# Performance work log

Hardware: AMD Instinct MI355X
Metric: run time of the kernel (lower is better)

## Reference

```python
import jax, jax.numpy as jnp
import numpy as np

N_EMBD = 2048
DIM_ATT = 2048
HEAD_SIZE = 64
N_HEAD = DIM_ATT // HEAD_SIZE
N_LAYER = 24
LAYER_ID = 12
CHUNK_LEN = 512
HEAD_DIV = 8
B = 4
TT = 4096


def _init_params():
    ratio_0_to_1 = LAYER_ID / (N_LAYER - 1)
    ratio_1_to_almost0 = 1.0 - LAYER_ID / N_LAYER
    ddd = (np.arange(N_EMBD) / N_EMBD).reshape(1, 1, N_EMBD).astype(np.float32)
    time_mix_k = np.power(ddd, ratio_1_to_almost0)
    time_mix_v = np.power(ddd, ratio_1_to_almost0) + 0.3 * ratio_0_to_1
    time_mix_r = np.power(ddd, 0.5 * ratio_1_to_almost0)
    time_mix_g = np.power(ddd, 0.5 * ratio_1_to_almost0)
    h = np.arange(N_HEAD, dtype=np.float32)
    time_decay = -8 + 7 * (h / (N_HEAD - 1)) ** (0.7 + 1.3 * ratio_0_to_1)
    time_faaaa = np.full(N_HEAD, 0.05, dtype=np.float32)
    return (jnp.asarray(time_mix_k), jnp.asarray(time_mix_v), jnp.asarray(time_mix_r),
            jnp.asarray(time_mix_g), jnp.asarray(time_decay.astype(np.float32)), jnp.asarray(time_faaaa))


def setup_inputs() -> dict:
    key = jax.random.key(0)
    ks = jax.random.split(key, 8)
    scale = 1.0 / np.sqrt(N_EMBD)
    x = jax.random.normal(ks[0], (B, TT, N_EMBD), dtype=jnp.float32)
    W_r = jax.random.normal(ks[1], (N_EMBD, DIM_ATT), dtype=jnp.float32) * scale
    W_k = jax.random.normal(ks[2], (N_EMBD, DIM_ATT), dtype=jnp.float32) * scale
    W_v = jax.random.normal(ks[3], (N_EMBD, DIM_ATT), dtype=jnp.float32) * scale
    W_g = jax.random.normal(ks[4], (N_EMBD, DIM_ATT), dtype=jnp.float32) * scale
    W_o = jax.random.normal(ks[5], (DIM_ATT, N_EMBD), dtype=jnp.float32) * scale
    ln_gamma = jnp.ones((DIM_ATT,), dtype=jnp.float32)
    ln_beta = jnp.zeros((DIM_ATT,), dtype=jnp.float32)
    tmk, tmv, tmr, tmg, tdecay, tfaaaa = _init_params()
    state0 = jnp.zeros((B, N_HEAD, HEAD_SIZE, HEAD_SIZE), dtype=jnp.float32)
    return dict(x=x, W_r=W_r, W_k=W_k, W_v=W_v, W_g=W_g, W_o=W_o,
                ln_gamma=ln_gamma, ln_beta=ln_beta,
                time_mix_k=tmk, time_mix_v=tmv, time_mix_r=tmr, time_mix_g=tmg,
                time_decay=tdecay, time_faaaa=tfaaaa, state0=state0)


def _group_norm(x, gamma, beta, num_groups, eps=1e-5):
    # x: [N, C]
    N, C = x.shape
    xg = x.reshape(N, num_groups, C // num_groups)
    mean = xg.mean(axis=-1, keepdims=True)
    var = xg.var(axis=-1, keepdims=True)
    xn = (xg - mean) * jax.lax.rsqrt(var + eps)
    return xn.reshape(N, C) * gamma + beta


def _decay_mats(time_decay, time_faaaa, T):
    w1 = jnp.exp(-jnp.exp(time_decay))[:, None]              # [H,1]
    u = time_faaaa[:, None]                                  # [H,1]
    ws = (w1 ** T).reshape(1, N_HEAD, 1, 1)                  # [1,H,1,1]
    ind = jnp.arange(T - 1, -1, -1, dtype=jnp.float32)[None, :]  # [1,T]
    w = w1 ** ind                                            # [H,T] decays T-1..0
    wk = w.reshape(1, N_HEAD, 1, T)
    wb = jnp.flip(wk, axis=-1).swapaxes(-2, -1)              # [1,H,T,1]
    wcat = jnp.concatenate([w[:, 1:], u], axis=1)            # [H,T]
    wpad = jnp.pad(wcat, ((0, 0), (0, T)))                   # [H,2T]
    wt = jnp.tile(wpad, (1, T))[:, :-T].reshape(N_HEAD, T, 2 * T - 1)
    wmat = wt[:, :, T - 1:].reshape(1, N_HEAD, T, T)         # intra-chunk matrix
    return wmat, wk, wb, ws


def reference(x, W_r, W_k, W_v, W_g, W_o, ln_gamma, ln_beta,
              time_mix_k, time_mix_v, time_mix_r, time_mix_g,
              time_decay, time_faaaa, state0):
    Bx, T_total, C = x.shape
    H, S = N_HEAD, HEAD_SIZE
    T = min(CHUNK_LEN, T_total)

    # time shift: prepend zeros (initial TimeShift state)
    xx = jnp.concatenate([jnp.zeros((Bx, 1, C), x.dtype), x[:, :-1, :]], axis=1)
    xk = x * time_mix_k + xx * (1 - time_mix_k)
    xv = x * time_mix_v + xx * (1 - time_mix_v)
    xr = x * time_mix_r + xx * (1 - time_mix_r)
    xg = x * time_mix_g + xx * (1 - time_mix_g)

    r = (xr @ W_r).reshape(Bx, T_total, H, S).transpose(0, 2, 1, 3)   # [B,H,TT,S]
    k = (xk @ W_k).reshape(Bx, T_total, H, S).transpose(0, 2, 3, 1)   # [B,H,S,TT]
    v = (xv @ W_v).reshape(Bx, T_total, H, S).transpose(0, 2, 1, 3)   # [B,H,TT,S]
    g = jax.nn.silu(xg @ W_g)                                         # [B,TT,C]

    wmat, wk, wb, ws = _decay_mats(time_decay, time_faaaa, T)
    wmat = wmat.astype(r.dtype); wk = wk.astype(r.dtype)
    wb = wb.astype(r.dtype); ws = ws.astype(r.dtype)

    nchunks = T_total // T
    # reshape into chunks: [nchunks, B, H, T, S]
    rc = r.reshape(Bx, H, nchunks, T, S).transpose(2, 0, 1, 3, 4)
    kc = k.reshape(Bx, H, S, nchunks, T).transpose(3, 0, 1, 2, 4)   # [n,B,H,S,T]
    vc = v.reshape(Bx, H, nchunks, T, S).transpose(2, 0, 1, 3, 4)

    def step(s, inp):
        rr, kk, vv = inp  # [B,H,T,S], [B,H,S,T], [B,H,T,S]
        att = (rr @ kk) * wmat                  # [B,H,T,T]
        out = att @ vv + (rr @ s) * wb          # [B,H,T,S]
        s_new = ws * s + (kk * wk) @ vv         # [B,H,S,S]
        return s_new, out

    s_final, xs = jax.lax.scan(step, state0.astype(r.dtype), (rc, kc, vc))
    # xs: [n,B,H,T,S] -> [B,H,TT,S]
    xout = xs.transpose(1, 2, 0, 3, 4).reshape(Bx, H, T_total, S)
    xout = xout.transpose(0, 2, 1, 3).reshape(Bx * T_total, H * S)
    xout = _group_norm(xout / HEAD_DIV, ln_gamma, ln_beta, H)
    xout = xout.reshape(Bx, T_total, H * S) * g
    return xout @ W_o
```

## Files before the change

kernel.cpp:

```cpp
#include <hip/hip_runtime.h>

typedef unsigned short u16;
typedef short short8 __attribute__((ext_vector_type(8)));
typedef float f32x4 __attribute__((ext_vector_type(4)));

struct __attribute__((aligned(8), may_alias)) U2 { unsigned int x, y; };
struct __attribute__((aligned(16), may_alias)) U4 { unsigned int x, y, z, w; };
struct __attribute__((aligned(16), may_alias)) F4 { float x, y, z, w; };

__device__ __forceinline__ float bf2f(u16 h) {
    union { unsigned int u; float f; } x; x.u = ((unsigned int)h) << 16; return x.f;
}
__device__ __forceinline__ u16 f2bf(float f) {
    union { float f; unsigned int u; } x; x.f = f;
    return (u16)((x.u + 0x7FFFu + ((x.u >> 16) & 1u)) >> 16);
}
__device__ __forceinline__ short8 lds8(const u16* p) {
    union { U2 q[2]; short8 s; } u;
    u.q[0] = *(const U2*)p;
    u.q[1] = *(const U2*)(p + 4);
    return u.s;
}
__device__ __forceinline__ void gl_lds16(const u16* g, u16* l) {
    __builtin_amdgcn_global_load_lds(
        (const __attribute__((address_space(1))) void*)g,
        (__attribute__((address_space(3))) void*)l, 16, 0, 0);
}

__global__ void transpose5(const float* __restrict__ s0, const float* __restrict__ s1,
                           const float* __restrict__ s2, const float* __restrict__ s3,
                           const float* __restrict__ s4,
                           u16* __restrict__ d0, u16* __restrict__ d1,
                           u16* __restrict__ d2, u16* __restrict__ d3,
                           u16* __restrict__ d4)
{
    const float* S; u16* D;
    switch (blockIdx.z) {
        case 0: S = s0; D = d0; break;
        case 1: S = s1; D = d1; break;
        case 2: S = s2; D = d2; break;
        case 3: S = s3; D = d3; break;
        default: S = s4; D = d4; break;
    }
    __shared__ float tile[32][33];
    int tx = threadIdx.x, ty = threadIdx.y;
    int bx = blockIdx.x * 32, by = blockIdx.y * 32;
    #pragma unroll
    for (int i = 0; i < 32; i += 8)
        tile[ty + i][tx] = S[(size_t)(by + ty + i) * 2048 + bx + tx];
    __syncthreads();
    #pragma unroll
    for (int i = 0; i < 32; i += 8)
        D[(size_t)(bx + ty + i) * 2048 + by + tx] = f2bf(tile[tx][ty + i]);
}

__global__ __launch_bounds__(256, 4) void mix_rows(
    const float* __restrict__ x, const float* __restrict__ tmix, u16* __restrict__ out)
{
    const int t = blockIdx.x;
    const int c = threadIdx.x * 8;
    const float* xp = x + (size_t)t * 2048 + c;
    const bool first = (t & 4095) == 0;
    F4 a0 = *(const F4*)xp, a1 = *(const F4*)(xp + 4);
    F4 p0 = {0.f, 0.f, 0.f, 0.f}, p1 = {0.f, 0.f, 0.f, 0.f};
    if (!first) { p0 = *(const F4*)(xp - 2048); p1 = *(const F4*)(xp - 2048 + 4); }
    F4 t0 = *(const F4*)(tmix + c), t1 = *(const F4*)(tmix + c + 4);
    float xc[8] = {a0.x, a0.y, a0.z, a0.w, a1.x, a1.y, a1.z, a1.w};
    float xq[8] = {p0.x, p0.y, p0.z, p0.w, p1.x, p1.y, p1.z, p1.w};
    float tm[8] = {t0.x, t0.y, t0.z, t0.w, t1.x, t1.y, t1.z, t1.w};
    union { u16 s[8]; U4 v; } ov;
    #pragma unroll
    for (int e = 0; e < 8; ++e)
        ov.s[e] = f2bf(xq[e] + tm[e] * (xc[e] - xq[e]));
    *(U4*)(out + (size_t)t * 2048 + c) = ov.v;
}

__device__ __forceinline__ void storeC(u16* p, float v) { *p = f2bf(v); }
__device__ __forceinline__ void storeC(float* p, float v) { *p = v; }

template <typename CT>
__global__ __launch_bounds__(256, 1) void gemm_bt(
    const u16* __restrict__ A, const u16* __restrict__ Bt, CT* __restrict__ C,
    int M, int N, int K)
{
    __shared__ u16 As[128][32];
    __shared__ u16 Bs[128][32];
    const int tid = threadIdx.x;
    const int lane = tid & 63, wv = tid >> 6;
    const int quad = lane >> 4, l16 = lane & 15;
    const int wm = (wv >> 1) * 64, wn = (wv & 1) * 64;
    const int bm = blockIdx.x * 128, bn = blockIdx.y * 128;

    const int sr = tid >> 2, ss = tid & 3;
    const u16* ga0 = A + (size_t)(bm + sr) * K + ss * 8;
    const u16* ga1 = A + (size_t)(bm + sr + 64) * K + ss * 8;
    const u16* gb0 = Bt + (size_t)(bn + sr) * K + ss * 8;
    const u16* gb1 = Bt + (size_t)(bn + sr + 64) * K + ss * 8;
    u16* la0 = &As[sr][ss * 8];
    u16* la1 = &As[sr + 64][ss * 8];
    u16* lb0 = &Bs[sr][ss * 8];
    u16* lb1 = &Bs[sr + 64][ss * 8];

    f32x4 acc[4][4];
    const f32x4 zero4 = {0.f, 0.f, 0.f, 0.f};
    #pragma unroll
    for (int i = 0; i < 4; ++i)
        #pragma unroll
        for (int j = 0; j < 4; ++j) acc[i][j] = zero4;

    for (int k0 = 0; k0 < K; k0 += 32) {
        __syncthreads();
        gl_lds16(ga0 + k0, la0);
        gl_lds16(ga1 + k0, la1);
        gl_lds16(gb0 + k0, lb0);
        gl_lds16(gb1 + k0, lb1);
        __syncthreads();
        short8 af[4], bfv[4];
        #pragma unroll
        for (int mt = 0; mt < 4; ++mt) af[mt] = lds8(&As[wm + mt * 16 + l16][quad * 8]);
        #pragma unroll
        for (int nt = 0; nt < 4; ++nt) bfv[nt] = lds8(&Bs[wn + nt * 16 + l16][quad * 8]);
        #pragma unroll
        for (int mt = 0; mt < 4; ++mt)
            #pragma unroll
            for (int nt = 0; nt < 4; ++nt)
                acc[mt][nt] = __builtin_amdgcn_mfma_f32_16x16x32_bf16(
                    af[mt], bfv[nt], acc[mt][nt], 0, 0, 0);
    }
    #pragma unroll
    for (int mt = 0; mt < 4; ++mt)
        #pragma unroll
        for (int nt = 0; nt < 4; ++nt)
            #pragma unroll
            for (int r = 0; r < 4; ++r) {
                int row = bm + wm + mt * 16 + quad * 4 + r;
                int col = bn + wn + nt * 16 + l16;
                storeC(&C[(size_t)row * N + col], acc[mt][nt][r]);
            }
}

__global__ __launch_bounds__(512, 1) void wkv_kernel(
    const u16* __restrict__ Rb, const u16* __restrict__ Kb,
    const u16* __restrict__ Vb, const u16* __restrict__ Gb,
    const float* __restrict__ td, const float* __restrict__ tf,
    const float* __restrict__ gamma, const float* __restrict__ beta,
    const float* __restrict__ st0, u16* __restrict__ Xout)
{
    __shared__ u16 kt[64][72];
    __shared__ u16 vtT[64][72];
    __shared__ u16 Pb[8][64][40];
    __shared__ float wpow[513];
    u16* stT = &Pb[0][0][0];

    const int blk = blockIdx.x;
    const int b = blk >> 5, h = blk & 31;
    const int tid = threadIdx.x;
    const int w = tid >> 6, lane = tid & 63;
    const int quad = lane >> 4, l16 = lane & 15;

    const float E = expf(td[h]);
    const float u = tf[h];
    for (int p = tid; p <= 512; p += 512) wpow[p] = expf(-(float)p * E);

    const int mtS = w >> 1;
    const int ntS0 = (w & 1) * 2;
    f32x4 stReg[2];
    {
        const float* sp = st0 + (((size_t)b * 32 + h) << 12);
        #pragma unroll
        for (int q = 0; q < 2; ++q)
            #pragma unroll
            for (int r = 0; r < 4; ++r) {
                int s1 = mtS * 16 + quad * 4 + r;
                int s2 = (ntS0 + q) * 16 + l16;
                stReg[q][r] = sp[s1 * 64 + s2];
            }
    }

    const size_t rowbase = ((size_t)b * 4096) * 2048 + (size_t)h * 64;
    const f32x4 zero4 = {0.f, 0.f, 0.f, 0.f};
    __syncthreads();

    for (int c = 0; c < 8; ++c) {
        const int t0 = c * 512;
        __syncthreads();
        #pragma unroll
        for (int q = 0; q < 2; ++q)
            #pragma unroll
            for (int r = 0; r < 4; ++r) {
                int s1 = mtS * 16 + quad * 4 + r;
                int s2 = (ntS0 + q) * 16 + l16;
                stT[s2 * 72 + s1] = f2bf(stReg[q][r]);
            }
        __syncthreads();

        short8 ar[4][2];
        #pragma unroll
        for (int mt = 0; mt < 4; ++mt)
            #pragma unroll
            for (int ks = 0; ks < 2; ++ks) {
                int t = t0 + w * 64 + mt * 16 + l16;
                const u16* p = Rb + rowbase + (size_t)t * 2048 + ks * 32 + quad * 8;
                union { U4 v; short8 s; } uu; uu.v = *(const U4*)p;
                ar[mt][ks] = uu.s;
            }

        f32x4 acc[4][4];
        #pragma unroll
        for (int i = 0; i < 4; ++i)
            #pragma unroll
            for (int j = 0; j < 4; ++j) acc[i][j] = zero4;
        #pragma unroll
        for (int ks = 0; ks < 2; ++ks)
            #pragma unroll
            for (int nt = 0; nt < 4; ++nt) {
                short8 bs = lds8(&stT[(nt * 16 + l16) * 72 + ks * 32 + quad * 8]);
                #pragma unroll
                for (int mt = 0; mt < 4; ++mt)
                    acc[mt][nt] = __builtin_amdgcn_mfma_f32_16x16x32_bf16(
                        ar[mt][ks], bs, acc[mt][nt], 0, 0, 0);
            }
        #pragma unroll
        for (int mt = 0; mt < 4; ++mt)
            #pragma unroll
            for (int r = 0; r < 4; ++r) {
                float f = wpow[w * 64 + mt * 16 + quad * 4 + r];
                #pragma unroll
                for (int nt = 0; nt < 4; ++nt) acc[mt][nt][r] *= f;
            }

        f32x4 sacc[2] = {zero4, zero4};

        for (int J = 0; J < 8; ++J) {
            __syncthreads();
            {
                int row = tid >> 3, seg = tid & 7;
                size_t goff = rowbase + (size_t)(t0 + J * 64 + row) * 2048 + seg * 8;
                union { U4 v; u16 s[8]; } kv, vv;
                kv.v = *(const U4*)(Kb + goff);
                vv.v = *(const U4*)(Vb + goff);
                *(U4*)&kt[row][seg * 8] = kv.v;
                #pragma unroll
                for (int e = 0; e < 8; ++e) vtT[seg * 8 + e][row] = vv.s[e];
            }
            __syncthreads();
            if (w >= J) {
                #pragma unroll
                for (int half = 0; half < 2; ++half) {
                    #pragma unroll
                    for (int jt2 = 0; jt2 < 2; ++jt2) {
                        int jt = half * 2 + jt2;
                        short8 bk0 = lds8(&kt[jt * 16 + l16][quad * 8]);
                        short8 bk1 = lds8(&kt[jt * 16 + l16][32 + quad * 8]);
                        #pragma unroll
                        for (int mt = 0; mt < 4; ++mt) {
                            f32x4 s4 = zero4;
                            s4 = __builtin_amdgcn_mfma_f32_16x16x32_bf16(ar[mt][0], bk0, s4, 0, 0, 0);
                            s4 = __builtin_amdgcn_mfma_f32_16x16x32_bf16(ar[mt][1], bk1, s4, 0, 0, 0);
                            int ibase = w * 64 + mt * 16 + quad * 4;
                            int j = J * 64 + jt * 16 + l16;
                            #pragma unroll
                            for (int r = 0; r < 4; ++r) {
                                int i = ibase + r;
                                float f = (j < i) ? wpow[i - j - 1] : ((j == i) ? u : 0.f);
                                Pb[w][mt * 16 + quad * 4 + r][jt2 * 16 + l16] = f2bf(s4[r] * f);
                            }
                        }
                    }
                    __builtin_amdgcn_wave_barrier();
                    short8 ap[4];
                    #pragma unroll
                    for (int mt = 0; mt < 4; ++mt)
                        ap[mt] = lds8(&Pb[w][mt * 16 + l16][quad * 8]);
                    #pragma unroll
                    for (int nt = 0; nt < 4; ++nt) {
                        short8 bv = lds8(&vtT[nt * 16 + l16][half * 32 + quad * 8]);
                        #pragma unroll
                        for (int mt = 0; mt < 4; ++mt)
                            acc[mt][nt] = __builtin_amdgcn_mfma_f32_16x16x32_bf16(
                                ap[mt], bv, acc[mt][nt], 0, 0, 0);
                    }
                }
            }
            {
                short8 aS[2];
                #pragma unroll
                for (int ks = 0; ks < 2; ++ks) {
                    union { short8 s; u16 us[8]; } t8;
                    #pragma unroll
                    for (int jj = 0; jj < 8; ++jj) {
                        int tl = ks * 32 + quad * 8 + jj;
                        float f = bf2f(kt[tl][mtS * 16 + l16]) * wpow[511 - (J * 64 + tl)];
                        t8.us[jj] = f2bf(f);
                    }
                    aS[ks] = t8.s;
                }
                #pragma unroll
                for (int q = 0; q < 2; ++q) {
                    short8 bv0 = lds8(&vtT[(ntS0 + q) * 16 + l16][quad * 8]);
                    short8 bv1 = lds8(&vtT[(ntS0 + q) * 16 + l16][32 + quad * 8]);
                    sacc[q] = __builtin_amdgcn_mfma_f32_16x16x32_bf16(aS[0], bv0, sacc[q], 0, 0, 0);
                    sacc[q] = __builtin_amdgcn_mfma_f32_16x16x32_bf16(aS[1], bv1, sacc[q], 0, 0, 0);
                }
            }
        }

        {
            float wsT = wpow[512];
            #pragma unroll
            for (int q = 0; q < 2; ++q)
                #pragma unroll
                for (int r = 0; r < 4; ++r)
                    stReg[q][r] = wsT * stReg[q][r] + sacc[q][r];
        }

        #pragma unroll
        for (int mt = 0; mt < 4; ++mt) {
            float rsum[4], rsq[4];
            #pragma unroll
            for (int r = 0; r < 4; ++r) {
                float s = 0.f, sq = 0.f;
                #pragma unroll
                for (int nt = 0; nt < 4; ++nt) {
                    float v = acc[mt][nt][r];
                    s += v; sq += v * v;
                }
                rsum[r] = s; rsq[r] = sq;
            }
            #pragma unroll
            for (int off = 1; off < 16; off <<= 1)
                #pragma unroll
                for (int r = 0; r < 4; ++r) {
                    rsum[r] += __shfl_xor(rsum[r], off);
                    rsq[r] += __shfl_xor(rsq[r], off);
                }
            #pragma unroll
            for (int r = 0; r < 4; ++r) {
                float mean = rsum[r] * (1.f / 512.f);
                float var = rsq[r] * (1.f / 4096.f) - mean * mean;
                float rstd = rsqrtf(var + 1e-5f);
                int tg = t0 + w * 64 + mt * 16 + quad * 4 + r;
                size_t obase = rowbase + (size_t)tg * 2048;
                #pragma unroll
                for (int nt = 0; nt < 4; ++nt) {
                    int ch = nt * 16 + l16;
                    float y = acc[mt][nt][r] * 0.125f;
                    float xn = (y - mean) * rstd * gamma[h * 64 + ch] + beta[h * 64 + ch];
                    float gl = bf2f(Gb[obase + ch]);
                    float sg = gl / (1.f + expf(-gl));
                    Xout[obase + ch] = f2bf(xn * sg);
                }
            }
        }
    }
}

extern "C" void kernel_launch(void* const* d_in, const int* in_sizes, int n_in,
                              void* d_out, int out_size, void* d_ws, size_t ws_size,
                              hipStream_t stream)
{
    const float* x   = (const float*)d_in[0];
    const float* Wr  = (const float*)d_in[1];
    const float* Wk  = (const float*)d_in[2];
    const float* Wv  = (const float*)d_in[3];
    const float* Wg  = (const float*)d_in[4];
    const float* Wo  = (const float*)d_in[5];
    const float* gam = (const float*)d_in[6];
    const float* bet = (const float*)d_in[7];
    const float* tmk = (const float*)d_in[8];
    const float* tmv = (const float*)d_in[9];
    const float* tmr = (const float*)d_in[10];
    const float* tmg = (const float*)d_in[11];
    const float* td  = (const float*)d_in[12];
    const float* tf  = (const float*)d_in[13];
    const float* st0 = (const float*)d_in[14];
    float* out = (float*)d_out;

    char* ws = (char*)d_ws;
    const size_t WSZ = (size_t)2048 * 2048 * 2;
    const size_t ASZ = (size_t)16384 * 2048 * 2;
    u16* WtR = (u16*)(ws + 0 * WSZ);
    u16* WtK = (u16*)(ws + 1 * WSZ);
    u16* WtV = (u16*)(ws + 2 * WSZ);
    u16* WtG = (u16*)(ws + 3 * WSZ);
    u16* WtO = (u16*)(ws + 4 * WSZ);
    char* act = ws + 5 * WSZ;
    u16* rb = (u16*)(act + 0 * ASZ);
    u16* kb = (u16*)(act + 1 * ASZ);
    u16* vb = (u16*)(act + 2 * ASZ);
    u16* gb = (u16*)(act + 3 * ASZ);
    u16* xo = gb;

    u16* mixA = (u16*)d_out;

    transpose5<<<dim3(64, 64, 5), dim3(32, 8), 0, stream>>>(
        Wr, Wk, Wv, Wg, Wo, WtR, WtK, WtV, WtG, WtO);

    dim3 ggrid(128, 16), gblk(256);
    dim3 mgrid(16384), mblk(256);

    mix_rows<<<mgrid, mblk, 0, stream>>>(x, tmr, mixA);
    gemm_bt<u16><<<ggrid, gblk, 0, stream>>>(mixA, WtR, rb, 16384, 2048, 2048);
    mix_rows<<<mgrid, mblk, 0, stream>>>(x, tmk, mixA);
    gemm_bt<u16><<<ggrid, gblk, 0, stream>>>(mixA, WtK, kb, 16384, 2048, 2048);
    mix_rows<<<mgrid, mblk, 0, stream>>>(x, tmv, mixA);
    gemm_bt<u16><<<ggrid, gblk, 0, stream>>>(mixA, WtV, vb, 16384, 2048, 2048);
    mix_rows<<<mgrid, mblk, 0, stream>>>(x, tmg, mixA);
    gemm_bt<u16><<<ggrid, gblk, 0, stream>>>(mixA, WtG, gb, 16384, 2048, 2048);

    wkv_kernel<<<dim3(128), dim3(512), 0, stream>>>(
        rb, kb, vb, gb, td, tf, gam, bet, st0, xo);

    gemm_bt<float><<<ggrid, gblk, 0, stream>>>(xo, WtO, out, 16384, 2048, 2048);
}
```

Before: 1.838 ms.

## Split WKV into chunk-parallel state, scan, and output kernels; pair mix kernels

The serial WKV kernel ran only 128 blocks (one per batch-head) that walked eight chunks in sequence. It is replaced by three kernels. The first computes each chunk's state contribution in parallel over 1024 blocks, the second runs a small scan that combines them with the initial state, and the third computes the chunk outputs in parallel over 1024 blocks. The aim is to fill the GPU instead of leaving most compute units idle during the recurrent section, at the cost of extra global traffic for the intermediate states. Separately, the token-shift mix kernels now produce two mixed inputs per launch, halving the reads of x.

```diff
diff --git a/kernel.cpp b/kernel.cpp
--- a/kernel.cpp
+++ b/kernel.cpp
@@ -54,8 +54,9 @@
         D[(size_t)(bx + ty + i) * 2048 + by + tx] = f2bf(tile[tx][ty + i]);
 }
 
-__global__ __launch_bounds__(256, 4) void mix_rows(
-    const float* __restrict__ x, const float* __restrict__ tmix, u16* __restrict__ out)
+__global__ __launch_bounds__(256, 4) void mix2_rows(
+    const float* __restrict__ x, const float* __restrict__ tmA,
+    const float* __restrict__ tmB, u16* __restrict__ outA, u16* __restrict__ outB)
 {
     const int t = blockIdx.x;
     const int c = threadIdx.x * 8;
@@ -64,15 +65,21 @@
     F4 a0 = *(const F4*)xp, a1 = *(const F4*)(xp + 4);
     F4 p0 = {0.f, 0.f, 0.f, 0.f}, p1 = {0.f, 0.f, 0.f, 0.f};
     if (!first) { p0 = *(const F4*)(xp - 2048); p1 = *(const F4*)(xp - 2048 + 4); }
-    F4 t0 = *(const F4*)(tmix + c), t1 = *(const F4*)(tmix + c + 4);
+    F4 ta0 = *(const F4*)(tmA + c), ta1 = *(const F4*)(tmA + c + 4);
+    F4 tb0 = *(const F4*)(tmB + c), tb1 = *(const F4*)(tmB + c + 4);
     float xc[8] = {a0.x, a0.y, a0.z, a0.w, a1.x, a1.y, a1.z, a1.w};
     float xq[8] = {p0.x, p0.y, p0.z, p0.w, p1.x, p1.y, p1.z, p1.w};
-    float tm[8] = {t0.x, t0.y, t0.z, t0.w, t1.x, t1.y, t1.z, t1.w};
-    union { u16 s[8]; U4 v; } ov;
-    #pragma unroll
-    for (int e = 0; e < 8; ++e)
-        ov.s[e] = f2bf(xq[e] + tm[e] * (xc[e] - xq[e]));
-    *(U4*)(out + (size_t)t * 2048 + c) = ov.v;
+    float ma[8] = {ta0.x, ta0.y, ta0.z, ta0.w, ta1.x, ta1.y, ta1.z, ta1.w};
+    float mb[8] = {tb0.x, tb0.y, tb0.z, tb0.w, tb1.x, tb1.y, tb1.z, tb1.w};
+    union { u16 s[8]; U4 v; } oa, ob;
+    #pragma unroll
+    for (int e = 0; e < 8; ++e) {
+        float d = xc[e] - xq[e];
+        oa.s[e] = f2bf(xq[e] + ma[e] * d);
+        ob.s[e] = f2bf(xq[e] + mb[e] * d);
+    }
+    *(U4*)(outA + (size_t)t * 2048 + c) = oa.v;
+    *(U4*)(outB + (size_t)t * 2048 + c) = ob.v;
 }
 
 __device__ __forceinline__ void storeC(u16* p, float v) { *p = f2bf(v); }
@@ -139,21 +146,114 @@
             }
 }
 
-__global__ __launch_bounds__(512, 1) void wkv_kernel(
+__global__ __launch_bounds__(256, 2) void wkv_state(
+    const u16* __restrict__ Kb, const u16* __restrict__ Vb,
+    const float* __restrict__ td, float* __restrict__ Sc)
+{
+    __shared__ u16 ktT[64][72];
+    __shared__ u16 vtT[64][72];
+    __shared__ float wpow[512];
+
+    const int blk = blockIdx.x;
+    const int c = blk & 7, h = (blk >> 3) & 31, b = blk >> 8;
+    const int tid = threadIdx.x;
+    const int w = tid >> 6, lane = tid & 63;
+    const int quad = lane >> 4, l16 = lane & 15;
+
+    const float E = expf(td[h]);
+    for (int p = tid; p < 512; p += 256) wpow[p] = expf(-(float)p * E);
+
+    const size_t rowbase = ((size_t)b * 4096 + c * 512) * 2048 + (size_t)h * 64;
+    const f32x4 zero4 = {0.f, 0.f, 0.f, 0.f};
+    f32x4 acc[4];
+    #pragma unroll
+    for (int nt = 0; nt < 4; ++nt) acc[nt] = zero4;
+    __syncthreads();
+
+    for (int J = 0; J < 8; ++J) {
+        __syncthreads();
+        #pragma unroll
+        for (int it = 0; it < 2; ++it) {
+            int slot = it * 256 + tid;
+            int row = slot >> 3, seg = slot & 7;
+            size_t goff = rowbase + (size_t)(J * 64 + row) * 2048 + seg * 8;
+            union { U4 v; u16 s[8]; } kv, vv;
+            kv.v = *(const U4*)(Kb + goff);
+            vv.v = *(const U4*)(Vb + goff);
+            float wp = wpow[511 - (J * 64 + row)];
+            #pragma unroll
+            for (int e = 0; e < 8; ++e) {
+                ktT[seg * 8 + e][row] = f2bf(bf2f(kv.s[e]) * wp);
+                vtT[seg * 8 + e][row] = vv.s[e];
+            }
+        }
+        __syncthreads();
+        short8 a0 = lds8(&ktT[w * 16 + l16][quad * 8]);
+        short8 a1 = lds8(&ktT[w * 16 + l16][32 + quad * 8]);
+        #pragma unroll
+        for (int nt = 0; nt < 4; ++nt) {
+            short8 b0 = lds8(&vtT[nt * 16 + l16][quad * 8]);
+            short8 b1 = lds8(&vtT[nt * 16 + l16][32 + quad * 8]);
+            acc[nt] = __builtin_amdgcn_mfma_f32_16x16x32_bf16(a0, b0, acc[nt], 0, 0, 0);
+            acc[nt] = __builtin_amdgcn_mfma_f32_16x16x32_bf16(a1, b1, acc[nt], 0, 0, 0);
+        }
+    }
+    float* out = Sc + ((size_t)((b * 32 + h) * 8 + c) << 12);
+    #pragma unroll
+    for (int nt = 0; nt < 4; ++nt)
+        #pragma unroll
+        for (int r = 0; r < 4; ++r)
+            out[(w * 16 + quad * 4 + r) * 64 + nt * 16 + l16] = acc[nt][r];
+}
+
+__global__ __launch_bounds__(256, 4) void wkv_scan(
+    const float* __restrict__ Sc, const float* __restrict__ st0,
+    const float* __restrict__ td, u16* __restrict__ SinT)
+{
+    const int blk = blockIdx.x;
+    const int h = blk & 31;
+    const int tid = threadIdx.x;
+    const int s2 = tid & 63;
+    const int s1b = (tid >> 6) * 16;
+    const float wsT = expf(-512.f * expf(td[h]));
+
+    float S[16];
+    const float* sp = st0 + ((size_t)blk << 12);
+    #pragma unroll
+    for (int i = 0; i < 16; ++i) S[i] = sp[(s1b + i) * 64 + s2];
+
+    const size_t base = ((size_t)blk * 8) << 12;
+    for (int c = 0; c < 8; ++c) {
+        u16* op = SinT + base + ((size_t)c << 12) + s2 * 64 + s1b;
+        union { u16 s[16]; U4 v[2]; } ov;
+        #pragma unroll
+        for (int i = 0; i < 16; ++i) ov.s[i] = f2bf(S[i]);
+        *(U4*)op = ov.v[0];
+        *(U4*)(op + 8) = ov.v[1];
+        if (c < 7) {
+            const float* cp = Sc + base + ((size_t)c << 12);
+            #pragma unroll
+            for (int i = 0; i < 16; ++i)
+                S[i] = wsT * S[i] + cp[(s1b + i) * 64 + s2];
+        }
+    }
+}
+
+__global__ __launch_bounds__(512, 1) void wkv_out(
     const u16* __restrict__ Rb, const u16* __restrict__ Kb,
     const u16* __restrict__ Vb, const u16* __restrict__ Gb,
+    const u16* __restrict__ SinT,
     const float* __restrict__ td, const float* __restrict__ tf,
     const float* __restrict__ gamma, const float* __restrict__ beta,
-    const float* __restrict__ st0, u16* __restrict__ Xout)
+    u16* __restrict__ Xout)
 {
     __shared__ u16 kt[64][72];
     __shared__ u16 vtT[64][72];
     __shared__ u16 Pb[8][64][40];
     __shared__ float wpow[513];
-    u16* stT = &Pb[0][0][0];
 
     const int blk = blockIdx.x;
-    const int b = blk >> 5, h = blk & 31;
+    const int c = blk & 7, h = (blk >> 3) & 31, b = blk >> 8;
     const int tid = threadIdx.x;
     const int w = tid >> 6, lane = tid & 63;
     const int quad = lane >> 4, l16 = lane & 15;
@@ -162,194 +262,136 @@
     const float u = tf[h];
     for (int p = tid; p <= 512; p += 512) wpow[p] = expf(-(float)p * E);
 
-    const int mtS = w >> 1;
-    const int ntS0 = (w & 1) * 2;
-    f32x4 stReg[2];
-    {
-        const float* sp = st0 + (((size_t)b * 32 + h) << 12);
-        #pragma unroll
-        for (int q = 0; q < 2; ++q)
-            #pragma unroll
-            for (int r = 0; r < 4; ++r) {
-                int s1 = mtS * 16 + quad * 4 + r;
-                int s2 = (ntS0 + q) * 16 + l16;
-                stReg[q][r] = sp[s1 * 64 + s2];
-            }
-    }
-
-    const size_t rowbase = ((size_t)b * 4096) * 2048 + (size_t)h * 64;
+    const size_t rowbase = ((size_t)b * 4096 + c * 512) * 2048 + (size_t)h * 64;
     const f32x4 zero4 = {0.f, 0.f, 0.f, 0.f};
     __syncthreads();
 
-    for (int c = 0; c < 8; ++c) {
-        const int t0 = c * 512;
-        __syncthreads();
-        #pragma unroll
-        for (int q = 0; q < 2; ++q)
-            #pragma unroll
-            for (int r = 0; r < 4; ++r) {
-                int s1 = mtS * 16 + quad * 4 + r;
-                int s2 = (ntS0 + q) * 16 + l16;
-                stT[s2 * 72 + s1] = f2bf(stReg[q][r]);
-            }
-        __syncthreads();
-
-        short8 ar[4][2];
-        #pragma unroll
-        for (int mt = 0; mt < 4; ++mt)
-            #pragma unroll
-            for (int ks = 0; ks < 2; ++ks) {
-                int t = t0 + w * 64 + mt * 16 + l16;
-                const u16* p = Rb + rowbase + (size_t)t * 2048 + ks * 32 + quad * 8;
-                union { U4 v; short8 s; } uu; uu.v = *(const U4*)p;
-                ar[mt][ks] = uu.s;
-            }
-
-        f32x4 acc[4][4];
-        #pragma unroll
-        for (int i = 0; i < 4; ++i)
-            #pragma unroll
-            for (int j = 0; j < 4; ++j) acc[i][j] = zero4;
-        #pragma unroll
-        for (int ks = 0; ks < 2; ++ks)
-            #pragma unroll
-            for (int nt = 0; nt < 4; ++nt) {
-                short8 bs = lds8(&stT[(nt * 16 + l16) * 72 + ks * 32 + quad * 8]);
+    short8 ar[4][2];
+    #pragma unroll
+    for (int mt = 0; mt < 4; ++mt)
+        #pragma unroll
+        for (int ks = 0; ks < 2; ++ks) {
+            int t = w * 64 + mt * 16 + l16;
+            const u16* p = Rb + rowbase + (size_t)t * 2048 + ks * 32 + quad * 8;
+            union { U4 v; short8 s; } uu; uu.v = *(const U4*)p;
+            ar[mt][ks] = uu.s;
+        }
+
+    const u16* sp = SinT + ((size_t)((b * 32 + h) * 8 + c) << 12);
+    f32x4 acc[4][4];
+    #pragma unroll
+    for (int i = 0; i < 4; ++i)
+        #pragma unroll
+        for (int j = 0; j < 4; ++j) acc[i][j] = zero4;
+    #pragma unroll
+    for (int ks = 0; ks < 2; ++ks)
+        #pragma unroll
+        for (int nt = 0; nt < 4; ++nt) {
+            union { U4 v; short8 s; } uu;
+            uu.v = *(const U4*)(sp + (nt * 16 + l16) * 64 + ks * 32 + quad * 8);
+            short8 bs = uu.s;
+            #pragma unroll
+            for (int mt = 0; mt < 4; ++mt)
+                acc[mt][nt] = __builtin_amdgcn_mfma_f32_16x16x32_bf16(
+                    ar[mt][ks], bs, acc[mt][nt], 0, 0, 0);
+        }
+    #pragma unroll
+    for (int mt = 0; mt < 4; ++mt)
+        #pragma unroll
+        for (int r = 0; r < 4; ++r) {
+            float f = wpow[w * 64 + mt * 16 + quad * 4 + r];
+            #pragma unroll
+            for (int nt = 0; nt < 4; ++nt) acc[mt][nt][r] *= f;
+        }
+
+    for (int J = 0; J < 8; ++J) {
+        __syncthreads();
+        {
+            int row = tid >> 3, seg = tid & 7;
+            size_t goff = rowbase + (size_t)(J * 64 + row) * 2048 + seg * 8;
+            union { U4 v; u16 s[8]; } kv, vv;
+            kv.v = *(const U4*)(Kb + goff);
+            vv.v = *(const U4*)(Vb + goff);
+            *(U4*)&kt[row][seg * 8] = kv.v;
+            #pragma unroll
+            for (int e = 0; e < 8; ++e) vtT[seg * 8 + e][row] = vv.s[e];
+        }
+        __syncthreads();
+        if (w >= J) {
+            #pragma unroll
+            for (int half = 0; half < 2; ++half) {
+                #pragma unroll
+                for (int jt2 = 0; jt2 < 2; ++jt2) {
+                    int jt = half * 2 + jt2;
+                    short8 bk0 = lds8(&kt[jt * 16 + l16][quad * 8]);
+                    short8 bk1 = lds8(&kt[jt * 16 + l16][32 + quad * 8]);
+                    #pragma unroll
+                    for (int mt = 0; mt < 4; ++mt) {
+                        f32x4 s4 = zero4;
+                        s4 = __builtin_amdgcn_mfma_f32_16x16x32_bf16(ar[mt][0], bk0, s4, 0, 0, 0);
+                        s4 = __builtin_amdgcn_mfma_f32_16x16x32_bf16(ar[mt][1], bk1, s4, 0, 0, 0);
+                        int ibase = w * 64 + mt * 16 + quad * 4;
+                        int j = J * 64 + jt * 16 + l16;
+                        #pragma unroll
+                        for (int r = 0; r < 4; ++r) {
+                            int i = ibase + r;
+                            float f = (j < i) ? wpow[i - j - 1] : ((j == i) ? u : 0.f);
+                            Pb[w][mt * 16 + quad * 4 + r][jt2 * 16 + l16] = f2bf(s4[r] * f);
+                        }
+                    }
+                }
+                __builtin_amdgcn_wave_barrier();
+                short8 ap[4];
                 #pragma unroll
                 for (int mt = 0; mt < 4; ++mt)
-                    acc[mt][nt] = __builtin_amdgcn_mfma_f32_16x16x32_bf16(
-                        ar[mt][ks], bs, acc[mt][nt], 0, 0, 0);
-            }
-        #pragma unroll
-        for (int mt = 0; mt < 4; ++mt)
-            #pragma unroll
-            for (int r = 0; r < 4; ++r) {
-                float f = wpow[w * 64 + mt * 16 + quad * 4 + r];
+                    ap[mt] = lds8(&Pb[w][mt * 16 + l16][quad * 8]);
                 #pragma unroll
-                for (int nt = 0; nt < 4; ++nt) acc[mt][nt][r] *= f;
-            }
-
-        f32x4 sacc[2] = {zero4, zero4};
-
-        for (int J = 0; J < 8; ++J) {
-            __syncthreads();
-            {
-                int row = tid >> 3, seg = tid & 7;
-                size_t goff = rowbase + (size_t)(t0 + J * 64 + row) * 2048 + seg * 8;
-                union { U4 v; u16 s[8]; } kv, vv;
-                kv.v = *(const U4*)(Kb + goff);
-                vv.v = *(const U4*)(Vb + goff);
-                *(U4*)&kt[row][seg * 8] = kv.v;
-                #pragma unroll
-                for (int e = 0; e < 8; ++e) vtT[seg * 8 + e][row] = vv.s[e];
-            }
-            __syncthreads();
-            if (w >= J) {
-                #pragma unroll
-                for (int half = 0; half < 2; ++half) {
-                    #pragma unroll
-                    for (int jt2 = 0; jt2 < 2; ++jt2) {
-                        int jt = half * 2 + jt2;
-                        short8 bk0 = lds8(&kt[jt * 16 + l16][quad * 8]);
-                        short8 bk1 = lds8(&kt[jt * 16 + l16][32 + quad * 8]);
-                        #pragma unroll
-                        for (int mt = 0; mt < 4; ++mt) {
-                            f32x4 s4 = zero4;
-                            s4 = __builtin_amdgcn_mfma_f32_16x16x32_bf16(ar[mt][0], bk0, s4, 0, 0, 0);
-                            s4 = __builtin_amdgcn_mfma_f32_16x16x32_bf16(ar[mt][1], bk1, s4, 0, 0, 0);
-                            int ibase = w * 64 + mt * 16 + quad * 4;
-                            int j = J * 64 + jt * 16 + l16;
-                            #pragma unroll
-                            for (int r = 0; r < 4; ++r) {
-                                int i = ibase + r;
-                                float f = (j < i) ? wpow[i - j - 1] : ((j == i) ? u : 0.f);
-                                Pb[w][mt * 16 + quad * 4 + r][jt2 * 16 + l16] = f2bf(s4[r] * f);
-                            }
-                        }
-                    }
-                    __builtin_amdgcn_wave_barrier();
-                    short8 ap[4];
+                for (int nt = 0; nt < 4; ++nt) {
+                    short8 bv = lds8(&vtT[nt * 16 + l16][half * 32 + quad * 8]);
                     #pragma unroll
                     for (int mt = 0; mt < 4; ++mt)
-                        ap[mt] = lds8(&Pb[w][mt * 16 + l16][quad * 8]);
-                    #pragma unroll
-                    for (int nt = 0; nt < 4; ++nt) {
-                        short8 bv = lds8(&vtT[nt * 16 + l16][half * 32 + quad * 8]);
-                        #pragma unroll
-                        for (int mt = 0; mt < 4; ++mt)
-                            acc[mt][nt] = __builtin_amdgcn_mfma_f32_16x16x32_bf16(
-                                ap[mt], bv, acc[mt][nt], 0, 0, 0);
-                    }
+                        acc[mt][nt] = __builtin_amdgcn_mfma_f32_16x16x32_bf16(
+                            ap[mt], bv, acc[mt][nt], 0, 0, 0);
                 }
             }
-            {
-                short8 aS[2];
-                #pragma unroll
-                for (int ks = 0; ks < 2; ++ks) {
-                    union { short8 s; u16 us[8]; } t8;
-                    #pragma unroll
-                    for (int jj = 0; jj < 8; ++jj) {
-                        int tl = ks * 32 + quad * 8 + jj;
-                        float f = bf2f(kt[tl][mtS * 16 + l16]) * wpow[511 - (J * 64 + tl)];
-                        t8.us[jj] = f2bf(f);
-                    }
-                    aS[ks] = t8.s;
-                }
-                #pragma unroll
-                for (int q = 0; q < 2; ++q) {
-                    short8 bv0 = lds8(&vtT[(ntS0 + q) * 16 + l16][quad * 8]);
-                    short8 bv1 = lds8(&vtT[(ntS0 + q) * 16 + l16][32 + quad * 8]);
-                    sacc[q] = __builtin_amdgcn_mfma_f32_16x16x32_bf16(aS[0], bv0, sacc[q], 0, 0, 0);
-                    sacc[q] = __builtin_amdgcn_mfma_f32_16x16x32_bf16(aS[1], bv1, sacc[q], 0, 0, 0);
-                }
-            }
-        }
-
-        {
-            float wsT = wpow[512];
-            #pragma unroll
-            for (int q = 0; q < 2; ++q)
-                #pragma unroll
-                for (int r = 0; r < 4; ++r)
-                    stReg[q][r] = wsT * stReg[q][r] + sacc[q][r];
-        }
-
-        #pragma unroll
-        for (int mt = 0; mt < 4; ++mt) {
-            float rsum[4], rsq[4];
+        }
+    }
+
+    #pragma unroll
+    for (int mt = 0; mt < 4; ++mt) {
+        float rsum[4], rsq[4];
+        #pragma unroll
+        for (int r = 0; r < 4; ++r) {
+            float s = 0.f, sq = 0.f;
+            #pragma unroll
+            for (int nt = 0; nt < 4; ++nt) {
+                float v = acc[mt][nt][r];
+                s += v; sq += v * v;
+            }
+            rsum[r] = s; rsq[r] = sq;
+        }
+        #pragma unroll
+        for (int off = 1; off < 16; off <<= 1)
             #pragma unroll
             for (int r = 0; r < 4; ++r) {
-                float s = 0.f, sq = 0.f;
-                #pragma unroll
-                for (int nt = 0; nt < 4; ++nt) {
-                    float v = acc[mt][nt][r];
-                    s += v; sq += v * v;
-                }
-                rsum[r] = s; rsq[r] = sq;
-            }
-            #pragma unroll
-            for (int off = 1; off < 16; off <<= 1)
-                #pragma unroll
-                for (int r = 0; r < 4; ++r) {
-                    rsum[r] += __shfl_xor(rsum[r], off);
-                    rsq[r] += __shfl_xor(rsq[r], off);
-                }
-            #pragma unroll
-            for (int r = 0; r < 4; ++r) {
-                float mean = rsum[r] * (1.f / 512.f);
-                float var = rsq[r] * (1.f / 4096.f) - mean * mean;
-                float rstd = rsqrtf(var + 1e-5f);
-                int tg = t0 + w * 64 + mt * 16 + quad * 4 + r;
-                size_t obase = rowbase + (size_t)tg * 2048;
-                #pragma unroll
-                for (int nt = 0; nt < 4; ++nt) {
-                    int ch = nt * 16 + l16;
-                    float y = acc[mt][nt][r] * 0.125f;
-                    float xn = (y - mean) * rstd * gamma[h * 64 + ch] + beta[h * 64 + ch];
-                    float gl = bf2f(Gb[obase + ch]);
-                    float sg = gl / (1.f + expf(-gl));
-                    Xout[obase + ch] = f2bf(xn * sg);
-                }
+                rsum[r] += __shfl_xor(rsum[r], off);
+                rsq[r] += __shfl_xor(rsq[r], off);
+            }
+        #pragma unroll
+        for (int r = 0; r < 4; ++r) {
+            float mean = rsum[r] * (1.f / 512.f);
+            float var = rsq[r] * (1.f / 4096.f) - mean * mean;
+            float rstd = rsqrtf(var + 1e-5f);
+            int tg = w * 64 + mt * 16 + quad * 4 + r;
+            size_t obase = rowbase + (size_t)tg * 2048;
+            #pragma unroll
+            for (int nt = 0; nt < 4; ++nt) {
+                int ch = nt * 16 + l16;
+                float y = acc[mt][nt][r] * 0.125f;
+                float xn = (y - mean) * rstd * gamma[h * 64 + ch] + beta[h * 64 + ch];
+                float gl = bf2f(Gb[obase + ch]);
+                float sg = gl / (1.f + expf(-gl));
+                Xout[obase + ch] = f2bf(xn * sg);
             }
         }
     }
@@ -392,6 +434,9 @@
     u16* xo = gb;
 
     u16* mixA = (u16*)d_out;
+    u16* mixB = (u16*)d_out + (size_t)16384 * 2048;
+    float* ScBuf = (float*)d_out;
+    u16* SinT = (u16*)((char*)d_out + (size_t)1024 * 4096 * 4);
 
     transpose5<<<dim3(64, 64, 5), dim3(32, 8), 0, stream>>>(
         Wr, Wk, Wv, Wg, Wo, WtR, WtK, WtV, WtG, WtO);
@@ -399,17 +444,17 @@
     dim3 ggrid(128, 16), gblk(256);
     dim3 mgrid(16384), mblk(256);
 
-    mix_rows<<<mgrid, mblk, 0, stream>>>(x, tmr, mixA);
+    mix2_rows<<<mgrid, mblk, 0, stream>>>(x, tmr, tmk, mixA, mixB);
     gemm_bt<u16><<<ggrid, gblk, 0, stream>>>(mixA, WtR, rb, 16384, 2048, 2048);
-    mix_rows<<<mgrid, mblk, 0, stream>>>(x, tmk, mixA);
-    gemm_bt<u16><<<ggrid, gblk, 0, stream>>>(mixA, WtK, kb, 16384, 2048, 2048);
-    mix_rows<<<mgrid, mblk, 0, stream>>>(x, tmv, mixA);
+    gemm_bt<u16><<<ggrid, gblk, 0, stream>>>(mixB, WtK, kb, 16384, 2048, 2048);
+    mix2_rows<<<mgrid, mblk, 0, stream>>>(x, tmv, tmg, mixA, mixB);
     gemm_bt<u16><<<ggrid, gblk, 0, stream>>>(mixA, WtV, vb, 16384, 2048, 2048);
-    mix_rows<<<mgrid, mblk, 0, stream>>>(x, tmg, mixA);
-    gemm_bt<u16><<<ggrid, gblk, 0, stream>>>(mixA, WtG, gb, 16384, 2048, 2048);
-
-    wkv_kernel<<<dim3(128), dim3(512), 0, stream>>>(
-        rb, kb, vb, gb, td, tf, gam, bet, st0, xo);
+    gemm_bt<u16><<<ggrid, gblk, 0, stream>>>(mixB, WtG, gb, 16384, 2048, 2048);
+
+    wkv_state<<<dim3(1024), dim3(256), 0, stream>>>(kb, vb, td, ScBuf);
+    wkv_scan<<<dim3(128), dim3(256), 0, stream>>>(ScBuf, st0, td, SinT);
+    wkv_out<<<dim3(1024), dim3(512), 0, stream>>>(
+        rb, kb, vb, gb, SinT, td, tf, gam, bet, xo);
 
     gemm_bt<float><<<ggrid, gblk, 0, stream>>>(xo, WtO, out, 16384, 2048, 2048);
 }
```

Result: faster. 1.608 ms (-12.5%).
